# Kernel optimization log

Measured on AMD Instinct MI355X. Metric: run time of the kernel, lower is better.

Reference implementation:

```python
import jax, jax.numpy as jnp
import numpy as np

S, B, H = 2048, 1, 1024
N_HEADS = 16
HEAD_DIM = H // N_HEADS
E, K, F = 8, 2, 2048  # experts, top_k, ffn_hidden
EPS = 1e-5


def layernorm(x, w, b):
    mu = jnp.mean(x, axis=-1, keepdims=True)
    var = jnp.mean(jnp.square(x - mu), axis=-1, keepdims=True)
    return (x - mu) * jax.lax.rsqrt(var + EPS) * w + b


def setup_inputs() -> dict:
    key = jax.random.key(0)
    ks = jax.random.split(key, 8)
    std = 0.02
    return {
        "x": jax.random.normal(ks[0], (S, B, H), dtype=jnp.float32),
        "ln1_w": jnp.ones((H,), jnp.float32),
        "ln1_b": jnp.zeros((H,), jnp.float32),
        "in_proj_w": jax.random.normal(ks[1], (3 * H, H), jnp.float32) * std,
        "in_proj_b": jnp.zeros((3 * H,), jnp.float32),
        "out_proj_w": jax.random.normal(ks[2], (H, H), jnp.float32) * std,
        "out_proj_b": jnp.zeros((H,), jnp.float32),
        "ln2_w": jnp.ones((H,), jnp.float32),
        "ln2_b": jnp.zeros((H,), jnp.float32),
        "router_w": jax.random.normal(ks[3], (E, H), jnp.float32) * std,
        "w1": jax.random.normal(ks[4], (E, H, F), jnp.float32) * std,
        "w2": jax.random.normal(ks[5], (E, F, H), jnp.float32) * std,
    }


def reference(x, ln1_w, ln1_b, in_proj_w, in_proj_b, out_proj_w, out_proj_b,
              ln2_w, ln2_b, router_w, w1, w2):
    s, b, h = x.shape
    # ---- causal self-attention (nn.MultiheadAttention math) ----
    hn = layernorm(x, ln1_w, ln1_b)
    qkv = hn @ in_proj_w.T + in_proj_b          # [S,B,3H]
    q, k, v = jnp.split(qkv, 3, axis=-1)
    q = q.reshape(s, b, N_HEADS, HEAD_DIM)
    k = k.reshape(s, b, N_HEADS, HEAD_DIM)
    v = v.reshape(s, b, N_HEADS, HEAD_DIM)
    scores = jnp.einsum('sbnd,tbnd->bnst', q, k) / np.sqrt(HEAD_DIM)
    causal = jnp.tril(jnp.ones((s, s), bool))
    scores = jnp.where(causal[None, None], scores, -jnp.inf)
    probs = jax.nn.softmax(scores, axis=-1)
    attn = jnp.einsum('bnst,tbnd->sbnd', probs, v).reshape(s, b, h)
    attn = attn @ out_proj_w.T + out_proj_b
    x1 = x + attn
    # ---- dMoE FFN: router softmax -> top-k gates -> expert GELU MLP ----
    hn2 = layernorm(x1, ln2_w, ln2_b).reshape(s * b, h)   # tokens [T,H]
    logits = hn2 @ router_w.T                              # [T,E]
    rp = jax.nn.softmax(logits, axis=-1)
    topw, topi = jax.lax.top_k(rp, K)                      # [T,K]
    gates = jnp.sum(jax.nn.one_hot(topi, E, dtype=hn2.dtype) * topw[..., None], axis=1)  # [T,E]
    hmid = jax.nn.gelu(jnp.einsum('th,ehf->tef', hn2, w1), approximate=False)  # [T,E,F]
    y = jnp.einsum('tef,efh->th', hmid * gates[:, :, None], w2)                # [T,H]
    return x1 + y.reshape(s, b, h)
```

## Files before the change

kernel.cpp:

```cpp
#include <hip/hip_runtime.h>

#define SL 2048
#define HID 1024
#define NHEAD 16
#define HD 64
#define NEXP 8
#define FF 2048
#define MAXTILE 40
#define MAXROWS (MAXTILE * 128)
#define CPAD 32

typedef short bf16x8 __attribute__((ext_vector_type(8)));
typedef float f32x4 __attribute__((ext_vector_type(4)));
typedef unsigned u32x4 __attribute__((ext_vector_type(4)));

__device__ __forceinline__ unsigned short f2bf(float f) {
  unsigned u = __builtin_bit_cast(unsigned, f);
  u += 0x7fffu + ((u >> 16) & 1u);
  return (unsigned short)(u >> 16);
}

__device__ __forceinline__ void gload16(const void* g, void* l) {
  __builtin_amdgcn_global_load_lds((const __attribute__((address_space(1))) void*)g,
                                   (__attribute__((address_space(3))) void*)l,
                                   16, 0, 0);
}

__device__ __forceinline__ void xcd_remap(int& bx, int& by) {
  const int nx = gridDim.x;
  const int nwg = nx * gridDim.y;
  const int L = by * nx + bx;
  const int per = nwg >> 3;
  const int Lp = (L & 7) * per + (L >> 3);
  bx = Lp % nx;
  by = Lp / nx;
}

#define PIPE_WAIT(i, NT)                                                     \
  if ((i) == (NT) - 1)                                                       \
    asm volatile("s_waitcnt vmcnt(0) lgkmcnt(0)" ::: "memory");              \
  else                                                                       \
    asm volatile("s_waitcnt vmcnt(4) lgkmcnt(0)" ::: "memory");              \
  __builtin_amdgcn_s_barrier();

#define GEMM_FRAGS_MFMA(CC)                                                  \
  bf16x8 af[4], bfr[4];                                                      \
  _Pragma("unroll")                                                          \
  for (int mt = 0; mt < 4; mt++)                                             \
    af[mt] = *reinterpret_cast<const bf16x8*>(                               \
        &Asm[CC][(wm + mt * 16 + la) * 32 + lk]);                            \
  _Pragma("unroll")                                                          \
  for (int nt = 0; nt < 4; nt++)                                             \
    bfr[nt] = *reinterpret_cast<const bf16x8*>(                              \
        &Bsm[CC][(wn + nt * 16 + la) * 32 + lk]);                            \
  __builtin_amdgcn_s_setprio(1);                                             \
  _Pragma("unroll")                                                          \
  for (int mt = 0; mt < 4; mt++)                                             \
    _Pragma("unroll")                                                        \
    for (int nt = 0; nt < 4; nt++)                                           \
      acc[mt][nt] =                                                          \
          __builtin_amdgcn_mfma_f32_16x16x32_bf16(af[mt], bfr[nt], acc[mt][nt], 0, 0, 0); \
  __builtin_amdgcn_s_setprio(0);

#define PIPE_ROT()                                                           \
  cc = (cc == 2) ? 0 : cc + 1;                                               \
  cs = (cs == 2) ? 0 : cs + 1;

template <int MODE>
__global__ __launch_bounds__(256) void gemm_bt(
    const unsigned short* __restrict__ A, const unsigned short* __restrict__ Bt,
    int M, int N, int Kstride, int Kloop,
    const float* __restrict__ bias,
    float* __restrict__ outf,
    unsigned short* __restrict__ q_out, unsigned short* __restrict__ k_out,
    unsigned short* __restrict__ vt_out)
{
  __shared__ unsigned short Asm[3][128 * 32];
  __shared__ unsigned short Bsm[3][128 * 32];
  int bx = blockIdx.x, by = blockIdx.y;
  xcd_remap(bx, by);
  const int tid = threadIdx.x;
  const int wave = tid >> 6;
  const int lane = tid & 63;
  const int m0 = by * 128;
  const int n0 = bx * 128;
  const int koff = blockIdx.z * Kloop;
  const int wm = (wave >> 1) * 64;
  const int wn = (wave & 1) * 64;
  const int la = lane & 15;
  const int lk = (lane >> 4) * 8;

  f32x4 acc[4][4] = {};

  const int srow = tid >> 2;
  const int skoff = (tid & 3) * 8;
  const unsigned short* Ag = A + (size_t)(m0 + srow) * Kstride + koff + skoff;
  const unsigned short* Bg = Bt + (size_t)(n0 + srow) * Kstride + koff + skoff;

  auto stage = [&](int s, int k0) {
    gload16(Ag + k0, &Asm[s][wave * 512]);
    gload16(Ag + (size_t)64 * Kstride + k0, &Asm[s][2048 + wave * 512]);
    gload16(Bg + k0, &Bsm[s][wave * 512]);
    gload16(Bg + (size_t)64 * Kstride + k0, &Bsm[s][2048 + wave * 512]);
  };

  stage(0, 0);
  stage(1, 32);
  const int NT = Kloop >> 5;
  int cc = 0, cs = 2;
  for (int i = 0; i < NT; ++i) {
    PIPE_WAIT(i, NT)
    if (i + 2 < NT) stage(cs, (i + 2) << 5);
    GEMM_FRAGS_MFMA(cc)
    PIPE_ROT()
  }

  const int lg = lane >> 4;
#pragma unroll
  for (int mt = 0; mt < 4; mt++) {
#pragma unroll
    for (int nt = 0; nt < 4; nt++) {
#pragma unroll
      for (int r = 0; r < 4; r++) {
        const int row = m0 + wm + mt * 16 + lg * 4 + r;
        const int col = n0 + wn + nt * 16 + la;
        float v = acc[mt][nt][r];
        if (MODE == 0) {
          v += bias[col];
          const int hh = (col & 1023) >> 6;
          const int dd = col & 63;
          const unsigned short bv = f2bf(v);
          if (col < 1024)
            q_out[(size_t)hh * SL * HD + (size_t)row * HD + dd] = bv;
          else if (col < 2048)
            k_out[(size_t)hh * SL * HD + (size_t)row * HD + dd] = bv;
          else
            vt_out[(size_t)hh * HD * SL + (size_t)dd * SL + row] = bv;
        } else {
          outf[(size_t)blockIdx.z * SL * HID + (size_t)row * HID + col] = v;
        }
      }
    }
  }
}

__global__ __launch_bounds__(256) void gemm_moe1(
    const unsigned short* __restrict__ A, const unsigned short* __restrict__ w1t,
    const int* __restrict__ perm, const float* __restrict__ gateg,
    const int* __restrict__ texp, const int* __restrict__ trow,
    unsigned short* __restrict__ hmidg)
{
  __shared__ unsigned short Asm[3][128 * 32];
  __shared__ unsigned short Bsm[3][128 * 32];
  int bx = blockIdx.x, by = blockIdx.y;
  xcd_remap(bx, by);
  const int e = texp[by];
  if (e < 0) return;
  const int row0 = trow[by];
  const int tid = threadIdx.x;
  const int wave = tid >> 6;
  const int lane = tid & 63;
  const int n0 = bx * 128;
  const int wm = (wave >> 1) * 64;
  const int wn = (wave & 1) * 64;
  const int la = lane & 15;
  const int lk = (lane >> 4) * 8;
  f32x4 acc[4][4] = {};

  const int srow = tid >> 2;
  const int skoff = (tid & 3) * 8;
  const int p0 = perm[row0 + srow];
  const int p1 = perm[row0 + 64 + srow];
  const unsigned short* Ag0 = A + (size_t)(p0 < 0 ? 0 : (p0 >> 1)) * HID + skoff;
  const unsigned short* Ag1 = A + (size_t)(p1 < 0 ? 0 : (p1 >> 1)) * HID + skoff;
  const unsigned short* Bg = w1t + (size_t)e * HID * FF + (size_t)(n0 + srow) * HID + skoff;

  auto stage = [&](int s, int k0) {
    gload16(Ag0 + k0, &Asm[s][wave * 512]);
    gload16(Ag1 + k0, &Asm[s][2048 + wave * 512]);
    gload16(Bg + k0, &Bsm[s][wave * 512]);
    gload16(Bg + (size_t)64 * HID + k0, &Bsm[s][2048 + wave * 512]);
  };

  stage(0, 0);
  stage(1, 32);
  const int NT = HID >> 5;
  int cc = 0, cs = 2;
  for (int i = 0; i < NT; ++i) {
    PIPE_WAIT(i, NT)
    if (i + 2 < NT) stage(cs, (i + 2) << 5);
    GEMM_FRAGS_MFMA(cc)
    PIPE_ROT()
  }

  const int lg = lane >> 4;
#pragma unroll
  for (int mt = 0; mt < 4; mt++) {
    float gr[4];
#pragma unroll
    for (int r = 0; r < 4; r++) gr[r] = gateg[row0 + wm + mt * 16 + lg * 4 + r];
#pragma unroll
    for (int nt = 0; nt < 4; nt++) {
#pragma unroll
      for (int r = 0; r < 4; r++) {
        const int grow = row0 + wm + mt * 16 + lg * 4 + r;
        const int col = n0 + wn + nt * 16 + la;
        const float v = acc[mt][nt][r];
        const float g = 0.5f * v * (1.0f + erff(v * 0.70710678118f));
        hmidg[(size_t)grow * FF + col] = f2bf(g * gr[r]);
      }
    }
  }
}

__global__ __launch_bounds__(256) void gemm_moe2(
    const unsigned short* __restrict__ A, const unsigned short* __restrict__ w2t,
    const int* __restrict__ perm,
    const int* __restrict__ texp, const int* __restrict__ trow,
    float* __restrict__ ybuf)
{
  __shared__ unsigned short Asm[3][128 * 32];
  __shared__ unsigned short Bsm[3][128 * 32];
  int bx = blockIdx.x, by = blockIdx.y;
  xcd_remap(bx, by);
  const int e = texp[by];
  if (e < 0) return;
  const int row0 = trow[by];
  const int tid = threadIdx.x;
  const int wave = tid >> 6;
  const int lane = tid & 63;
  const int n0 = bx * 128;
  const int koff = blockIdx.z * (FF / 2);
  const int wm = (wave >> 1) * 64;
  const int wn = (wave & 1) * 64;
  const int la = lane & 15;
  const int lk = (lane >> 4) * 8;
  f32x4 acc[4][4] = {};

  const int srow = tid >> 2;
  const int skoff = (tid & 3) * 8;
  const unsigned short* Ag = A + (size_t)(row0 + srow) * FF + koff + skoff;
  const unsigned short* Bg = w2t + (size_t)e * FF * HID + (size_t)(n0 + srow) * FF + koff + skoff;

  auto stage = [&](int s, int k0) {
    gload16(Ag + k0, &Asm[s][wave * 512]);
    gload16(Ag + (size_t)64 * FF + k0, &Asm[s][2048 + wave * 512]);
    gload16(Bg + k0, &Bsm[s][wave * 512]);
    gload16(Bg + (size_t)64 * FF + k0, &Bsm[s][2048 + wave * 512]);
  };

  stage(0, 0);
  stage(1, 32);
  const int NT = (FF / 2) >> 5;
  int cc = 0, cs = 2;
  for (int i = 0; i < NT; ++i) {
    PIPE_WAIT(i, NT)
    if (i + 2 < NT) stage(cs, (i + 2) << 5);
    GEMM_FRAGS_MFMA(cc)
    PIPE_ROT()
  }

  const int lg = lane >> 4;
#pragma unroll
  for (int mt = 0; mt < 4; mt++) {
    int pr[4];
#pragma unroll
    for (int r = 0; r < 4; r++) pr[r] = perm[row0 + wm + mt * 16 + lg * 4 + r];
#pragma unroll
    for (int nt = 0; nt < 4; nt++) {
#pragma unroll
      for (int r = 0; r < 4; r++) {
        const int p = pr[r];
        if (p >= 0) {
          const int col = n0 + wn + nt * 16 + la;
          ybuf[(size_t)(blockIdx.z * 2 + (p & 1)) * SL * HID + (size_t)(p >> 1) * HID + col] =
              acc[mt][nt][r];
        }
      }
    }
  }
}

__global__ __launch_bounds__(256) void ln_kernel(
    const float* __restrict__ x, const float* __restrict__ w, const float* __restrict__ b,
    unsigned short* __restrict__ ob)
{
  const int row = blockIdx.x;
  const int tid = threadIdx.x;
  const float4 v = *reinterpret_cast<const float4*>(&x[(size_t)row * HID + tid * 4]);
  float s = v.x + v.y + v.z + v.w;
  float q = v.x * v.x + v.y * v.y + v.z * v.z + v.w * v.w;
  for (int off = 32; off > 0; off >>= 1) {
    s += __shfl_down(s, off);
    q += __shfl_down(q, off);
  }
  __shared__ float ps[4], pq[4];
  const int wave = tid >> 6, lane = tid & 63;
  if (lane == 0) { ps[wave] = s; pq[wave] = q; }
  __syncthreads();
  s = ps[0] + ps[1] + ps[2] + ps[3];
  q = pq[0] + pq[1] + pq[2] + pq[3];
  const float mu = s * (1.0f / HID);
  const float inv = rsqrtf(q * (1.0f / HID) - mu * mu + 1e-5f);
  const int i = tid * 4;
  const float4 wv = *reinterpret_cast<const float4*>(&w[i]);
  const float4 bv = *reinterpret_cast<const float4*>(&b[i]);
  ushort4 u;
  u.x = f2bf((v.x - mu) * inv * wv.x + bv.x);
  u.y = f2bf((v.y - mu) * inv * wv.y + bv.y);
  u.z = f2bf((v.z - mu) * inv * wv.z + bv.z);
  u.w = f2bf((v.w - mu) * inv * wv.w + bv.w);
  *reinterpret_cast<ushort4*>(&ob[(size_t)row * HID + i]) = u;
}

__global__ __launch_bounds__(256) void combine_ln(
    const float4* __restrict__ x, const float* __restrict__ bias,
    const float4* __restrict__ p0, const float4* __restrict__ p1,
    float4* __restrict__ x1,
    const float* __restrict__ w, const float* __restrict__ b,
    unsigned short* __restrict__ ob, float* __restrict__ of)
{
  const int row = blockIdx.x;
  const int tid = threadIdx.x;
  const int i4 = row * 256 + tid;
  const int i = tid * 4;
  const float4 bv0 = *reinterpret_cast<const float4*>(&bias[i]);
  const float4 a = x[i4], c = p0[i4], d = p1[i4];
  float4 v;
  v.x = a.x + bv0.x + c.x + d.x;
  v.y = a.y + bv0.y + c.y + d.y;
  v.z = a.z + bv0.z + c.z + d.z;
  v.w = a.w + bv0.w + c.w + d.w;
  x1[i4] = v;
  float s = v.x + v.y + v.z + v.w;
  float q = v.x * v.x + v.y * v.y + v.z * v.z + v.w * v.w;
  for (int off = 32; off > 0; off >>= 1) {
    s += __shfl_down(s, off);
    q += __shfl_down(q, off);
  }
  __shared__ float ps[4], pq[4];
  const int wave = tid >> 6, lane = tid & 63;
  if (lane == 0) { ps[wave] = s; pq[wave] = q; }
  __syncthreads();
  s = ps[0] + ps[1] + ps[2] + ps[3];
  q = pq[0] + pq[1] + pq[2] + pq[3];
  const float mu = s * (1.0f / HID);
  const float inv = rsqrtf(q * (1.0f / HID) - mu * mu + 1e-5f);
  const float4 wv = *reinterpret_cast<const float4*>(&w[i]);
  const float4 bv = *reinterpret_cast<const float4*>(&b[i]);
  const float o0 = (v.x - mu) * inv * wv.x + bv.x;
  const float o1 = (v.y - mu) * inv * wv.y + bv.y;
  const float o2 = (v.z - mu) * inv * wv.z + bv.z;
  const float o3 = (v.w - mu) * inv * wv.w + bv.w;
  ushort4 u; u.x = f2bf(o0); u.y = f2bf(o1); u.z = f2bf(o2); u.w = f2bf(o3);
  *reinterpret_cast<ushort4*>(&ob[(size_t)row * HID + i]) = u;
  float4 o; o.x = o0; o.y = o1; o.z = o2; o.w = o3;
  *reinterpret_cast<float4*>(&of[(size_t)row * HID + i]) = o;
}

__global__ __launch_bounds__(256) void transpose_all(
    const float* __restrict__ w1, const float* __restrict__ w2,
    unsigned short* __restrict__ w1t, unsigned short* __restrict__ w2t)
{
  __shared__ unsigned lt[128 * 66];
  const int z = blockIdx.z;
  const float* in;
  unsigned short* out;
  int R, C, r0, c0;
  if (z < 8) {
    in = w1 + (size_t)z * HID * FF;  out = w1t + (size_t)z * HID * FF;
    R = HID; C = FF;  r0 = blockIdx.y * 128;  c0 = blockIdx.x * 128;
  } else {
    in = w2 + (size_t)(z - 8) * FF * HID;  out = w2t + (size_t)(z - 8) * FF * HID;
    R = FF; C = HID;  r0 = blockIdx.x * 128;  c0 = blockIdx.y * 128;
  }
  const int tid = threadIdx.x;
#pragma unroll
  for (int it = 0; it < 8; it++) {
    const int idx = it * 256 + tid;
    const int rp = idx >> 5;
    const int c4 = (idx & 31) * 4;
    const int r = rp * 2;
    const float4 v0 = *reinterpret_cast<const float4*>(&in[(size_t)(r0 + r) * C + c0 + c4]);
    const float4 v1 = *reinterpret_cast<const float4*>(&in[(size_t)(r0 + r + 1) * C + c0 + c4]);
    const int s = ((c4 >> 2) & 7) << 1;
    const int ri = rp ^ s;
    lt[(c4 + 0) * 66 + ri] = (unsigned)f2bf(v0.x) | ((unsigned)f2bf(v1.x) << 16);
    lt[(c4 + 1) * 66 + ri] = (unsigned)f2bf(v0.y) | ((unsigned)f2bf(v1.y) << 16);
    lt[(c4 + 2) * 66 + ri] = (unsigned)f2bf(v0.z) | ((unsigned)f2bf(v1.z) << 16);
    lt[(c4 + 3) * 66 + ri] = (unsigned)f2bf(v0.w) | ((unsigned)f2bf(v1.w) << 16);
  }
  __syncthreads();
#pragma unroll
  for (int it = 0; it < 16; it++) {
    const int idx = it * 256 + tid;
    const int c = idx >> 5;
    const int r4 = (idx & 31) * 4;
    const int s = ((c >> 2) & 7) << 1;
    const unsigned u0 = lt[c * 66 + ((r4 >> 1) ^ s)];
    const unsigned u1 = lt[c * 66 + (((r4 >> 1) + 1) ^ s)];
    ushort4 u;
    u.x = (unsigned short)(u0 & 0xffff);
    u.y = (unsigned short)(u0 >> 16);
    u.z = (unsigned short)(u1 & 0xffff);
    u.w = (unsigned short)(u1 >> 16);
    *reinterpret_cast<ushort4*>(&out[(size_t)(c0 + c) * R + r0 + r4]) = u;
  }
}

__global__ __launch_bounds__(256) void conv_bf16_2(
    const float4* __restrict__ a, const float4* __restrict__ b,
    ushort4* __restrict__ oa, ushort4* __restrict__ ob, int na4, int nb4)
{
  const int i = blockIdx.x * 256 + threadIdx.x;
  if (i < na4) {
    const float4 v = a[i];
    ushort4 u; u.x = f2bf(v.x); u.y = f2bf(v.y); u.z = f2bf(v.z); u.w = f2bf(v.w);
    oa[i] = u;
  } else if (i - na4 < nb4) {
    const float4 v = b[i - na4];
    ushort4 u; u.x = f2bf(v.x); u.y = f2bf(v.y); u.z = f2bf(v.z); u.w = f2bf(v.w);
    ob[i - na4] = u;
  }
}

__global__ __launch_bounds__(256) void router_kernel(
    const float* __restrict__ hn2f, const float* __restrict__ rw,
    int* __restrict__ ti, float* __restrict__ tg, int* __restrict__ cnt)
{
  __shared__ float wlds[NEXP * HID];
  __shared__ int lcnt[NEXP];
  const int tid = threadIdx.x;
#pragma unroll
  for (int i = 0; i < 8; i++)
    *reinterpret_cast<float4*>(&wlds[i * 1024 + tid * 4]) =
        *reinterpret_cast<const float4*>(&rw[i * 1024 + tid * 4]);
  if (tid < NEXP) lcnt[tid] = 0;
  __syncthreads();

  const int wave = tid >> 6, lane = tid & 63;
#pragma unroll 1
  for (int k = 0; k < 4; k++) {
    const int t = blockIdx.x * 16 + wave * 4 + k;
    float4 xr[4];
#pragma unroll
    for (int c = 0; c < 4; c++)
      xr[c] = *reinterpret_cast<const float4*>(&hn2f[(size_t)t * HID + c * 256 + lane * 4]);
    float p[NEXP];
#pragma unroll
    for (int e = 0; e < NEXP; e++) {
      float s = 0.f;
#pragma unroll
      for (int c = 0; c < 4; c++) {
        const float4 wv = *reinterpret_cast<const float4*>(&wlds[e * 1024 + c * 256 + lane * 4]);
        s += xr[c].x * wv.x + xr[c].y * wv.y + xr[c].z * wv.z + xr[c].w * wv.w;
      }
      s += __shfl_xor(s, 32);
      s += __shfl_xor(s, 16);
      s += __shfl_xor(s, 8);
      s += __shfl_xor(s, 4);
      s += __shfl_xor(s, 2);
      s += __shfl_xor(s, 1);
      p[e] = s;
    }
    if (lane == 0) {
      float mx = p[0];
#pragma unroll
      for (int e = 1; e < NEXP; e++) mx = fmaxf(mx, p[e]);
      float Z = 0.f;
#pragma unroll
      for (int e = 0; e < NEXP; e++) { p[e] = expf(p[e] - mx); Z += p[e]; }
      const float invZ = 1.f / Z;
      int i1 = 0;
#pragma unroll
      for (int e = 1; e < NEXP; e++) if (p[e] > p[i1]) i1 = e;
      int i2 = (i1 == 0) ? 1 : 0;
#pragma unroll
      for (int e = 0; e < NEXP; e++) if (e != i1 && p[e] > p[i2]) i2 = e;
      ti[2 * t] = i1; ti[2 * t + 1] = i2;
      tg[2 * t] = p[i1] * invZ; tg[2 * t + 1] = p[i2] * invZ;
      atomicAdd(&lcnt[i1], 1);
      atomicAdd(&lcnt[i2], 1);
    }
  }
  __syncthreads();
  if (tid < NEXP && lcnt[tid] > 0) atomicAdd(&cnt[tid * CPAD], lcnt[tid]);
}

__global__ void scan_kernel(const int* __restrict__ cnt, int* __restrict__ poff,
                            int* __restrict__ texp, int* __restrict__ trow)
{
  if (threadIdx.x == 0 && blockIdx.x == 0) {
    int off = 0, nt = 0;
    for (int e = 0; e < NEXP; e++) {
      poff[e] = off;
      const int c = cnt[e * CPAD];
      const int ntl = (c + 127) >> 7;
      for (int i = 0; i < ntl; i++) { texp[nt] = e; trow[nt] = off + i * 128; nt++; }
      off += ntl * 128;
    }
    for (int i = nt; i < MAXTILE; i++) { texp[i] = -1; trow[i] = 0; }
  }
}

__global__ __launch_bounds__(256) void build_kernel(
    const int* __restrict__ ti, const float* __restrict__ tg,
    const int* __restrict__ poff, int* __restrict__ fill,
    int* __restrict__ perm, float* __restrict__ gateg)
{
  __shared__ int lcnt[NEXP], lbase[NEXP];
  const int tid = threadIdx.x;
  if (tid < NEXP) lcnt[tid] = 0;
  __syncthreads();
  const int t = blockIdx.x * 256 + tid;
  int e0 = ti[2 * t], e1 = ti[2 * t + 1];
  int l0 = atomicAdd(&lcnt[e0], 1);
  int l1 = atomicAdd(&lcnt[e1], 1);
  __syncthreads();
  if (tid < NEXP) lbase[tid] = (lcnt[tid] > 0) ? atomicAdd(&fill[tid * CPAD], lcnt[tid]) : 0;
  __syncthreads();
  int pos0 = poff[e0] + lbase[e0] + l0;
  int pos1 = poff[e1] + lbase[e1] + l1;
  perm[pos0] = 2 * t;
  gateg[pos0] = tg[2 * t];
  perm[pos1] = 2 * t + 1;
  gateg[pos1] = tg[2 * t + 1];
}

__global__ __launch_bounds__(256) void final_add(
    const float4* __restrict__ x1, const float4* __restrict__ y0,
    const float4* __restrict__ y1, const float4* __restrict__ y2,
    const float4* __restrict__ y3, float4* __restrict__ out)
{
  const int i = blockIdx.x * 256 + threadIdx.x;
  const float4 a = x1[i], b = y0[i], c = y1[i], d = y2[i], e = y3[i];
  float4 o;
  o.x = a.x + b.x + c.x + d.x + e.x;
  o.y = a.y + b.y + c.y + d.y + e.y;
  o.z = a.z + b.z + c.z + d.z + e.z;
  o.w = a.w + b.w + c.w + d.w + e.w;
  out[i] = o;
}

#define SC2 0.1803368801111204f
#define PPITCH 20
__global__ __launch_bounds__(512) void attn_kernel(
    const unsigned short* __restrict__ qb, const unsigned short* __restrict__ kb,
    const unsigned short* __restrict__ vtb, unsigned short* __restrict__ attn)
{
  const int h = blockIdx.y;
  const int tid = threadIdx.x;
  const int wave = tid >> 6, lane = tid & 63;
  const int grp = wave >> 2;
  const int w4 = wave & 3;
  const int la = lane & 15, lg = lane >> 4;
  const int la7 = la & 7;
  __shared__ unsigned short Kt[2][2][64 * 64];
  __shared__ unsigned short Vt[2][2][64 * 64];
  __shared__ unsigned plds[8 * 32 * PPITCH];
  const unsigned short* qh = qb + (size_t)h * SL * HD;
  const unsigned short* kh = kb + (size_t)h * SL * HD;
  const unsigned short* vh = vtb + (size_t)h * HD * SL;
  unsigned* pu = &plds[wave * 32 * PPITCH];

  const int sr_lo = w4 * 8 + (lane >> 3);
  const int ss = lane & 7;

  auto stageKV = [&](int t, int buf) {
    const int kvb = t * 64;
#pragma unroll
    for (int j = 0; j < 2; j++) {
      const int row = j * 32 + sr_lo;
      const int s = ss ^ (row & 7);
      gload16(kh + (size_t)(kvb + row) * HD + s * 8, &Kt[grp][buf][j * 2048 + w4 * 512]);
      gload16(vh + (size_t)row * SL + kvb + s * 8, &Vt[grp][buf][j * 2048 + w4 * 512]);
    }
  };

  for (int half = 0; half < 2; half++) {
    const int qt = half ? (31 - blockIdx.x) : blockIdx.x;
    const int m0 = qt * 64 + w4 * 16;
    const int T = qt + 1;
    const int S = (T + 1) >> 1;
    const int q = m0 + la;

    bf16x8 aq0 = *reinterpret_cast<const bf16x8*>(&qh[(size_t)(m0 + la) * HD + lg * 8]);
    bf16x8 aq1 = *reinterpret_cast<const bf16x8*>(&qh[(size_t)(m0 + la) * HD + 32 + lg * 8]);

    f32x4 oacc[4] = {};
    float mrun = -1e30f, lrun = 0.f;

    if (grp < T) stageKV(grp, 0);
    __syncthreads();
    int cur = 0;

    for (int s = 0; s < S; s++) {
      const int tmy = 2 * s + grp;
      if (tmy + 2 < T) stageKV(tmy + 2, cur ^ 1);
      if (tmy < T) {
        const int kv0 = tmy * 64;
        const unsigned short* Kb = Kt[grp][cur];
        const unsigned short* Vb = Vt[grp][cur];

        f32x4 sac[4] = {};
        __builtin_amdgcn_s_setprio(1);
#pragma unroll
        for (int nt = 0; nt < 4; nt++) {
          const int row = nt * 16 + la;
          bf16x8 b0 = *reinterpret_cast<const bf16x8*>(&Kb[row * 64 + ((lg ^ la7) << 3)]);
          bf16x8 b1 = *reinterpret_cast<const bf16x8*>(&Kb[row * 64 + (((4 + lg) ^ la7) << 3)]);
          sac[nt] = __builtin_amdgcn_mfma_f32_16x16x32_bf16(b0, aq0, sac[nt], 0, 0, 0);
          sac[nt] = __builtin_amdgcn_mfma_f32_16x16x32_bf16(b1, aq1, sac[nt], 0, 0, 0);
        }
        __builtin_amdgcn_s_setprio(0);
        float sv[4][4];
        const bool diag = (tmy == qt);
#pragma unroll
        for (int nt = 0; nt < 4; nt++)
#pragma unroll
          for (int r = 0; r < 4; r++) {
            float xs = sac[nt][r] * SC2;
            if (diag && (kv0 + nt * 16 + lg * 4 + r) > q) xs = -1e30f;
            sv[nt][r] = xs;
          }
        float pm = fmaxf(fmaxf(sv[0][0], sv[0][1]), fmaxf(sv[0][2], sv[0][3]));
#pragma unroll
        for (int nt = 1; nt < 4; nt++)
          pm = fmaxf(pm, fmaxf(fmaxf(sv[nt][0], sv[nt][1]), fmaxf(sv[nt][2], sv[nt][3])));
        pm = fmaxf(pm, __shfl_xor(pm, 16));
        pm = fmaxf(pm, __shfl_xor(pm, 32));
        const float mn = fmaxf(mrun, pm);
        float rs = 0.f;
#pragma unroll
        for (int nt = 0; nt < 4; nt++)
#pragma unroll
          for (int r = 0; r < 4; r++) {
            const float pe = exp2f(sv[nt][r] - mn);
            sv[nt][r] = pe;
            rs += pe;
          }
        rs += __shfl_xor(rs, 16);
        rs += __shfl_xor(rs, 32);
        if (__ballot(pm > mrun) != 0ULL) {
          const float al = exp2f(mrun - mn);
#pragma unroll
          for (int dt = 0; dt < 4; dt++)
#pragma unroll
            for (int r = 0; r < 4; r++) oacc[dt][r] *= al;
          lrun = lrun * al + rs;
          mrun = mn;
        } else {
          lrun += rs;
        }
#pragma unroll
        for (int nt = 0; nt < 4; nt++)
#pragma unroll
          for (int rp = 0; rp < 2; rp++) {
            unsigned pk;
            asm("v_cvt_pk_bf16_f32 %0, %1, %2"
                : "=v"(pk) : "v"(sv[nt][rp * 2]), "v"(sv[nt][rp * 2 + 1]));
            pu[(nt * 8 + lg * 2 + rp) * PPITCH + la] = pk;
          }
        asm volatile("s_waitcnt lgkmcnt(0)" ::: "memory");
        __builtin_amdgcn_sched_barrier(0);
        u32x4 w0, w1;
#pragma unroll
        for (int jj = 0; jj < 4; jj++) {
          w0[jj] = pu[(lg * 4 + jj) * PPITCH + la];
          w1[jj] = pu[(16 + lg * 4 + jj) * PPITCH + la];
        }
        const bf16x8 pa0 = __builtin_bit_cast(bf16x8, w0);
        const bf16x8 pa1 = __builtin_bit_cast(bf16x8, w1);
        __builtin_amdgcn_s_setprio(1);
#pragma unroll
        for (int dt = 0; dt < 4; dt++) {
          const int row = dt * 16 + la;
          bf16x8 v0 = *reinterpret_cast<const bf16x8*>(&Vb[row * 64 + ((lg ^ la7) << 3)]);
          bf16x8 v1 = *reinterpret_cast<const bf16x8*>(&Vb[row * 64 + (((4 + lg) ^ la7) << 3)]);
          oacc[dt] = __builtin_amdgcn_mfma_f32_16x16x32_bf16(v0, pa0, oacc[dt], 0, 0, 0);
          oacc[dt] = __builtin_amdgcn_mfma_f32_16x16x32_bf16(v1, pa1, oacc[dt], 0, 0, 0);
        }
        __builtin_amdgcn_s_setprio(0);
      }
      __syncthreads();
      cur ^= 1;
    }

    float* xb = (float*)&Kt[0][0][0];
    float* mlb = (float*)&Vt[0][0][0];
    if (grp == 1) {
#pragma unroll
      for (int dt = 0; dt < 4; dt++)
#pragma unroll
        for (int r = 0; r < 4; r++)
          xb[w4 * 1024 + (dt * 16 + lg * 4 + r) * 16 + la] = oacc[dt][r];
      if (lg == 0) {
        mlb[w4 * 32 + la * 2] = mrun;
        mlb[w4 * 32 + la * 2 + 1] = lrun;
      }
    }
    __syncthreads();
    if (grp == 0) {
      const float m1 = mlb[w4 * 32 + la * 2];
      const float l1 = mlb[w4 * 32 + la * 2 + 1];
      const float mm = fmaxf(mrun, m1);
      const float a0 = exp2f(mrun - mm);
      const float a1 = exp2f(m1 - mm);
      const float linv = 1.0f / (lrun * a0 + l1 * a1);
#pragma unroll
      for (int dt = 0; dt < 4; dt++) {
        ushort4 u;
        float o0 = (oacc[dt][0] * a0 + xb[w4 * 1024 + (dt * 16 + lg * 4 + 0) * 16 + la] * a1) * linv;
        float o1 = (oacc[dt][1] * a0 + xb[w4 * 1024 + (dt * 16 + lg * 4 + 1) * 16 + la] * a1) * linv;
        float o2 = (oacc[dt][2] * a0 + xb[w4 * 1024 + (dt * 16 + lg * 4 + 2) * 16 + la] * a1) * linv;
        float o3 = (oacc[dt][3] * a0 + xb[w4 * 1024 + (dt * 16 + lg * 4 + 3) * 16 + la] * a1) * linv;
        u.x = f2bf(o0); u.y = f2bf(o1); u.z = f2bf(o2); u.w = f2bf(o3);
        *reinterpret_cast<ushort4*>(&attn[(size_t)q * HID + h * HD + dt * 16 + lg * 4]) = u;
      }
    }
    __syncthreads();
  }
}

extern "C" void kernel_launch(void* const* d_in, const int* in_sizes, int n_in,
                              void* d_out, int out_size, void* d_ws, size_t ws_size,
                              hipStream_t stream)
{
  const float* x          = (const float*)d_in[0];
  const float* ln1_w      = (const float*)d_in[1];
  const float* ln1_b      = (const float*)d_in[2];
  const float* in_proj_w  = (const float*)d_in[3];
  const float* in_proj_b  = (const float*)d_in[4];
  const float* out_proj_w = (const float*)d_in[5];
  const float* out_proj_b = (const float*)d_in[6];
  const float* ln2_w      = (const float*)d_in[7];
  const float* ln2_b      = (const float*)d_in[8];
  const float* router_w   = (const float*)d_in[9];
  const float* w1         = (const float*)d_in[10];
  const float* w2         = (const float*)d_in[11];
  float* out = (float*)d_out;

  char* ws = (char*)d_ws;
  size_t off = 0;
  auto alloc = [&](size_t bytes) -> void* {
    void* p = ws + off;
    off += (bytes + 255) & ~(size_t)255;
    return p;
  };
  unsigned short* hn_b   = (unsigned short*)alloc((size_t)SL * HID * 2);
  unsigned short* ipw_b  = (unsigned short*)alloc((size_t)3 * HID * HID * 2);
  unsigned short* opw_b  = (unsigned short*)alloc((size_t)HID * HID * 2);
  unsigned short* qb     = (unsigned short*)alloc((size_t)SL * HID * 2);
  unsigned short* kb     = (unsigned short*)alloc((size_t)SL * HID * 2);
  unsigned short* vtb    = (unsigned short*)alloc((size_t)SL * HID * 2);
  unsigned short* attn_b = (unsigned short*)alloc((size_t)SL * HID * 2);
  float*          x1     = (float*)alloc((size_t)SL * HID * 4);
  float*          pbuf   = (float*)alloc((size_t)2 * SL * HID * 4);
  unsigned short* hn2_b  = (unsigned short*)alloc((size_t)SL * HID * 2);
  float*          hn2_f  = (float*)alloc((size_t)SL * HID * 4);
  unsigned short* w1t    = (unsigned short*)alloc((size_t)NEXP * HID * FF * 2);
  unsigned short* w2t    = (unsigned short*)alloc((size_t)NEXP * HID * FF * 2);
  unsigned short* hmidg  = (unsigned short*)alloc((size_t)MAXROWS * FF * 2);
  float*          ybuf   = (float*)alloc((size_t)4 * SL * HID * 4);
  int*            ti     = (int*)alloc((size_t)SL * 2 * 4);
  float*          tg     = (float*)alloc((size_t)SL * 2 * 4);
  int*            perm   = (int*)alloc((size_t)MAXROWS * 4);
  float*          gateg  = (float*)alloc((size_t)MAXROWS * 4);
  int*            cnt    = (int*)alloc(NEXP * CPAD * 4);
  int*            fill   = (int*)alloc(NEXP * CPAD * 4);
  int*            poff   = (int*)alloc(64 * 4);
  int*            texp   = (int*)alloc(64 * 4);
  int*            trow   = (int*)alloc(64 * 4);

  const dim3 blk(256);

  hipMemsetAsync(cnt, 0, NEXP * CPAD * 4, stream);
  hipMemsetAsync(fill, 0, NEXP * CPAD * 4, stream);
  hipMemsetAsync(perm, 0xFF, (size_t)MAXROWS * 4, stream);
  hipMemsetAsync(gateg, 0, (size_t)MAXROWS * 4, stream);

  conv_bf16_2<<<4096, blk, 0, stream>>>(
      (const float4*)in_proj_w, (const float4*)out_proj_w,
      (ushort4*)ipw_b, (ushort4*)opw_b, 3 * HID * HID / 4, HID * HID / 4);
  transpose_all<<<dim3(16, 8, 16), blk, 0, stream>>>(w1, w2, w1t, w2t);

  ln_kernel<<<SL, blk, 0, stream>>>(x, ln1_w, ln1_b, hn_b);

  gemm_bt<0><<<dim3(3 * HID / 128, SL / 128), blk, 0, stream>>>(
      hn_b, ipw_b, SL, 3 * HID, HID, HID,
      in_proj_b, nullptr, qb, kb, vtb);

  attn_kernel<<<dim3(16, NHEAD), dim3(512), 0, stream>>>(qb, kb, vtb, attn_b);

  gemm_bt<2><<<dim3(HID / 128, SL / 128, 2), blk, 0, stream>>>(
      attn_b, opw_b, SL, HID, HID, HID / 2,
      nullptr, pbuf, nullptr, nullptr, nullptr);

  combine_ln<<<SL, blk, 0, stream>>>(
      (const float4*)x, out_proj_b, (const float4*)pbuf,
      (const float4*)(pbuf + (size_t)SL * HID), (float4*)x1,
      ln2_w, ln2_b, hn2_b, hn2_f);

  router_kernel<<<SL / 16, blk, 0, stream>>>(hn2_f, router_w, ti, tg, cnt);
  scan_kernel<<<1, 64, 0, stream>>>(cnt, poff, texp, trow);
  build_kernel<<<SL / 256, blk, 0, stream>>>(ti, tg, poff, fill, perm, gateg);

  gemm_moe1<<<dim3(FF / 128, MAXTILE), blk, 0, stream>>>(
      hn2_b, w1t, perm, gateg, texp, trow, hmidg);
  gemm_moe2<<<dim3(HID / 128, MAXTILE, 2), blk, 0, stream>>>(
      hmidg, w2t, perm, texp, trow, ybuf);

  final_add<<<SL * HID / 1024, blk, 0, stream>>>(
      (const float4*)x1, (const float4*)ybuf,
      (const float4*)(ybuf + (size_t)SL * HID),
      (const float4*)(ybuf + (size_t)2 * SL * HID),
      (const float4*)(ybuf + (size_t)3 * SL * HID),
      (float4*)out);
}
```

Baseline: 266.1 us.

## Fuse weight conversion into LN1 and expert transpose into QKV GEMM launch

```diff
diff --git a/kernel.cpp b/kernel.cpp
--- a/kernel.cpp
+++ b/kernel.cpp
@@ -66,14 +66,137 @@
   cc = (cc == 2) ? 0 : cc + 1;                                               \
   cs = (cs == 2) ? 0 : cs + 1;
 
+__global__ __launch_bounds__(256) void qkv_trans_kernel(
+    const unsigned short* __restrict__ A, const unsigned short* __restrict__ Bt,
+    const float* __restrict__ bias,
+    unsigned short* __restrict__ q_out, unsigned short* __restrict__ k_out,
+    unsigned short* __restrict__ vt_out,
+    const float* __restrict__ w1, const float* __restrict__ w2,
+    unsigned short* __restrict__ w1t, unsigned short* __restrict__ w2t)
+{
+  __shared__ union {
+    struct { unsigned short A[3][4096]; unsigned short B[3][4096]; } g;
+    unsigned lt[128 * 66];
+  } sm;
+  const int tid = threadIdx.x;
+
+  if (blockIdx.z == 0) {
+    unsigned short (*Asm)[4096] = sm.g.A;
+    unsigned short (*Bsm)[4096] = sm.g.B;
+    int bx = blockIdx.x, by = blockIdx.y;
+    xcd_remap(bx, by);
+    const int wave = tid >> 6;
+    const int lane = tid & 63;
+    const int m0 = by * 128;
+    const int n0 = bx * 128;
+    const int wm = (wave >> 1) * 64;
+    const int wn = (wave & 1) * 64;
+    const int la = lane & 15;
+    const int lk = (lane >> 4) * 8;
+
+    f32x4 acc[4][4] = {};
+
+    const int srow = tid >> 2;
+    const int skoff = (tid & 3) * 8;
+    const unsigned short* Ag = A + (size_t)(m0 + srow) * HID + skoff;
+    const unsigned short* Bg = Bt + (size_t)(n0 + srow) * HID + skoff;
+
+    auto stage = [&](int s, int k0) {
+      gload16(Ag + k0, &Asm[s][wave * 512]);
+      gload16(Ag + (size_t)64 * HID + k0, &Asm[s][2048 + wave * 512]);
+      gload16(Bg + k0, &Bsm[s][wave * 512]);
+      gload16(Bg + (size_t)64 * HID + k0, &Bsm[s][2048 + wave * 512]);
+    };
+
+    stage(0, 0);
+    stage(1, 32);
+    const int NT = HID >> 5;
+    int cc = 0, cs = 2;
+    for (int i = 0; i < NT; ++i) {
+      PIPE_WAIT(i, NT)
+      if (i + 2 < NT) stage(cs, (i + 2) << 5);
+      GEMM_FRAGS_MFMA(cc)
+      PIPE_ROT()
+    }
+
+    const int lg = lane >> 4;
+#pragma unroll
+    for (int mt = 0; mt < 4; mt++) {
+#pragma unroll
+      for (int nt = 0; nt < 4; nt++) {
+#pragma unroll
+        for (int r = 0; r < 4; r++) {
+          const int row = m0 + wm + mt * 16 + lg * 4 + r;
+          const int col = n0 + wn + nt * 16 + la;
+          float v = acc[mt][nt][r] + bias[col];
+          const int hh = (col & 1023) >> 6;
+          const int dd = col & 63;
+          const unsigned short bv = f2bf(v);
+          if (col < 1024)
+            q_out[(size_t)hh * SL * HD + (size_t)row * HD + dd] = bv;
+          else if (col < 2048)
+            k_out[(size_t)hh * SL * HD + (size_t)row * HD + dd] = bv;
+          else
+            vt_out[(size_t)hh * HD * SL + (size_t)dd * SL + row] = bv;
+        }
+      }
+    }
+  } else {
+    const int id = blockIdx.y * 24 + blockIdx.x;
+    if (id >= 256) return;
+    const int tx = id & 15;
+    const int ty = (id >> 4) & 7;
+    const int tz = ((int)blockIdx.z - 1) * 2 + (id >> 7);
+    const float* in;
+    unsigned short* out;
+    int R, C, r0, c0;
+    if (tz < 8) {
+      in = w1 + (size_t)tz * HID * FF;  out = w1t + (size_t)tz * HID * FF;
+      R = HID; C = FF;  r0 = ty * 128;  c0 = tx * 128;
+    } else {
+      in = w2 + (size_t)(tz - 8) * FF * HID;  out = w2t + (size_t)(tz - 8) * FF * HID;
+      R = FF; C = HID;  r0 = tx * 128;  c0 = ty * 128;
+    }
+#pragma unroll
+    for (int it = 0; it < 8; it++) {
+      const int idx = it * 256 + tid;
+      const int rp = idx >> 5;
+      const int c4 = (idx & 31) * 4;
+      const int r = rp * 2;
+      const float4 v0 = *reinterpret_cast<const float4*>(&in[(size_t)(r0 + r) * C + c0 + c4]);
+      const float4 v1 = *reinterpret_cast<const float4*>(&in[(size_t)(r0 + r + 1) * C + c0 + c4]);
+      const int s = ((c4 >> 2) & 7) << 1;
+      const int ri = rp ^ s;
+      sm.lt[(c4 + 0) * 66 + ri] = (unsigned)f2bf(v0.x) | ((unsigned)f2bf(v1.x) << 16);
+      sm.lt[(c4 + 1) * 66 + ri] = (unsigned)f2bf(v0.y) | ((unsigned)f2bf(v1.y) << 16);
+      sm.lt[(c4 + 2) * 66 + ri] = (unsigned)f2bf(v0.z) | ((unsigned)f2bf(v1.z) << 16);
+      sm.lt[(c4 + 3) * 66 + ri] = (unsigned)f2bf(v0.w) | ((unsigned)f2bf(v1.w) << 16);
+    }
+    __syncthreads();
+#pragma unroll
+    for (int it = 0; it < 16; it++) {
+      const int idx = it * 256 + tid;
+      const int c = idx >> 5;
+      const int r4 = (idx & 31) * 4;
+      const int s = ((c >> 2) & 7) << 1;
+      const unsigned u0 = sm.lt[c * 66 + ((r4 >> 1) ^ s)];
+      const unsigned u1 = sm.lt[c * 66 + (((r4 >> 1) + 1) ^ s)];
+      ushort4 u;
+      u.x = (unsigned short)(u0 & 0xffff);
+      u.y = (unsigned short)(u0 >> 16);
+      u.z = (unsigned short)(u1 & 0xffff);
+      u.w = (unsigned short)(u1 >> 16);
+      *reinterpret_cast<ushort4*>(&out[(size_t)(c0 + c) * R + r0 + r4]) = u;
+    }
+  }
+}
+
 template <int MODE>
 __global__ __launch_bounds__(256) void gemm_bt(
     const unsigned short* __restrict__ A, const unsigned short* __restrict__ Bt,
     int M, int N, int Kstride, int Kloop,
     const float* __restrict__ bias,
-    float* __restrict__ outf,
-    unsigned short* __restrict__ q_out, unsigned short* __restrict__ k_out,
-    unsigned short* __restrict__ vt_out)
+    float* __restrict__ outf)
 {
   __shared__ unsigned short Asm[3][128 * 32];
   __shared__ unsigned short Bsm[3][128 * 32];
@@ -124,21 +247,7 @@
       for (int r = 0; r < 4; r++) {
         const int row = m0 + wm + mt * 16 + lg * 4 + r;
         const int col = n0 + wn + nt * 16 + la;
-        float v = acc[mt][nt][r];
-        if (MODE == 0) {
-          v += bias[col];
-          const int hh = (col & 1023) >> 6;
-          const int dd = col & 63;
-          const unsigned short bv = f2bf(v);
-          if (col < 1024)
-            q_out[(size_t)hh * SL * HD + (size_t)row * HD + dd] = bv;
-          else if (col < 2048)
-            k_out[(size_t)hh * SL * HD + (size_t)row * HD + dd] = bv;
-          else
-            vt_out[(size_t)hh * HD * SL + (size_t)dd * SL + row] = bv;
-        } else {
-          outf[(size_t)blockIdx.z * SL * HID + (size_t)row * HID + col] = v;
-        }
+        outf[(size_t)blockIdx.z * SL * HID + (size_t)row * HID + col] = acc[mt][nt][r];
       }
     }
   }
@@ -281,36 +390,53 @@
   }
 }
 
-__global__ __launch_bounds__(256) void ln_kernel(
+__global__ __launch_bounds__(256) void ln_conv_kernel(
     const float* __restrict__ x, const float* __restrict__ w, const float* __restrict__ b,
-    unsigned short* __restrict__ ob)
-{
-  const int row = blockIdx.x;
+    unsigned short* __restrict__ ob,
+    const float4* __restrict__ cva, const float4* __restrict__ cvb,
+    ushort4* __restrict__ coa, ushort4* __restrict__ cob)
+{
   const int tid = threadIdx.x;
-  const float4 v = *reinterpret_cast<const float4*>(&x[(size_t)row * HID + tid * 4]);
-  float s = v.x + v.y + v.z + v.w;
-  float q = v.x * v.x + v.y * v.y + v.z * v.z + v.w * v.w;
-  for (int off = 32; off > 0; off >>= 1) {
-    s += __shfl_down(s, off);
-    q += __shfl_down(q, off);
-  }
-  __shared__ float ps[4], pq[4];
-  const int wave = tid >> 6, lane = tid & 63;
-  if (lane == 0) { ps[wave] = s; pq[wave] = q; }
-  __syncthreads();
-  s = ps[0] + ps[1] + ps[2] + ps[3];
-  q = pq[0] + pq[1] + pq[2] + pq[3];
-  const float mu = s * (1.0f / HID);
-  const float inv = rsqrtf(q * (1.0f / HID) - mu * mu + 1e-5f);
-  const int i = tid * 4;
-  const float4 wv = *reinterpret_cast<const float4*>(&w[i]);
-  const float4 bv = *reinterpret_cast<const float4*>(&b[i]);
-  ushort4 u;
-  u.x = f2bf((v.x - mu) * inv * wv.x + bv.x);
-  u.y = f2bf((v.y - mu) * inv * wv.y + bv.y);
-  u.z = f2bf((v.z - mu) * inv * wv.z + bv.z);
-  u.w = f2bf((v.w - mu) * inv * wv.w + bv.w);
-  *reinterpret_cast<ushort4*>(&ob[(size_t)row * HID + i]) = u;
+  if ((int)blockIdx.x < SL) {
+    const int row = blockIdx.x;
+    const float4 v = *reinterpret_cast<const float4*>(&x[(size_t)row * HID + tid * 4]);
+    float s = v.x + v.y + v.z + v.w;
+    float q = v.x * v.x + v.y * v.y + v.z * v.z + v.w * v.w;
+    for (int off = 32; off > 0; off >>= 1) {
+      s += __shfl_down(s, off);
+      q += __shfl_down(q, off);
+    }
+    __shared__ float ps[4], pq[4];
+    const int wave = tid >> 6, lane = tid & 63;
+    if (lane == 0) { ps[wave] = s; pq[wave] = q; }
+    __syncthreads();
+    s = ps[0] + ps[1] + ps[2] + ps[3];
+    q = pq[0] + pq[1] + pq[2] + pq[3];
+    const float mu = s * (1.0f / HID);
+    const float inv = rsqrtf(q * (1.0f / HID) - mu * mu + 1e-5f);
+    const int i = tid * 4;
+    const float4 wv = *reinterpret_cast<const float4*>(&w[i]);
+    const float4 bv = *reinterpret_cast<const float4*>(&b[i]);
+    ushort4 u;
+    u.x = f2bf((v.x - mu) * inv * wv.x + bv.x);
+    u.y = f2bf((v.y - mu) * inv * wv.y + bv.y);
+    u.z = f2bf((v.z - mu) * inv * wv.z + bv.z);
+    u.w = f2bf((v.w - mu) * inv * wv.w + bv.w);
+    *reinterpret_cast<ushort4*>(&ob[(size_t)row * HID + i]) = u;
+  } else {
+    const int NA = 3 * HID * HID / 4, NB = HID * HID / 4;
+    for (int i = ((int)blockIdx.x - SL) * 256 + tid; i < NA + NB; i += 512 * 256) {
+      if (i < NA) {
+        const float4 v = cva[i];
+        ushort4 u; u.x = f2bf(v.x); u.y = f2bf(v.y); u.z = f2bf(v.z); u.w = f2bf(v.w);
+        coa[i] = u;
+      } else {
+        const float4 v = cvb[i - NA];
+        ushort4 u; u.x = f2bf(v.x); u.y = f2bf(v.y); u.z = f2bf(v.z); u.w = f2bf(v.w);
+        cob[i - NA] = u;
+      }
+    }
+  }
 }
 
 __global__ __launch_bounds__(256) void combine_ln(
@@ -356,72 +482,6 @@
   *reinterpret_cast<ushort4*>(&ob[(size_t)row * HID + i]) = u;
   float4 o; o.x = o0; o.y = o1; o.z = o2; o.w = o3;
   *reinterpret_cast<float4*>(&of[(size_t)row * HID + i]) = o;
-}
-
-__global__ __launch_bounds__(256) void transpose_all(
-    const float* __restrict__ w1, const float* __restrict__ w2,
-    unsigned short* __restrict__ w1t, unsigned short* __restrict__ w2t)
-{
-  __shared__ unsigned lt[128 * 66];
-  const int z = blockIdx.z;
-  const float* in;
-  unsigned short* out;
-  int R, C, r0, c0;
-  if (z < 8) {
-    in = w1 + (size_t)z * HID * FF;  out = w1t + (size_t)z * HID * FF;
-    R = HID; C = FF;  r0 = blockIdx.y * 128;  c0 = blockIdx.x * 128;
-  } else {
-    in = w2 + (size_t)(z - 8) * FF * HID;  out = w2t + (size_t)(z - 8) * FF * HID;
-    R = FF; C = HID;  r0 = blockIdx.x * 128;  c0 = blockIdx.y * 128;
-  }
-  const int tid = threadIdx.x;
-#pragma unroll
-  for (int it = 0; it < 8; it++) {
-    const int idx = it * 256 + tid;
-    const int rp = idx >> 5;
-    const int c4 = (idx & 31) * 4;
-    const int r = rp * 2;
-    const float4 v0 = *reinterpret_cast<const float4*>(&in[(size_t)(r0 + r) * C + c0 + c4]);
-    const float4 v1 = *reinterpret_cast<const float4*>(&in[(size_t)(r0 + r + 1) * C + c0 + c4]);
-    const int s = ((c4 >> 2) & 7) << 1;
-    const int ri = rp ^ s;
-    lt[(c4 + 0) * 66 + ri] = (unsigned)f2bf(v0.x) | ((unsigned)f2bf(v1.x) << 16);
-    lt[(c4 + 1) * 66 + ri] = (unsigned)f2bf(v0.y) | ((unsigned)f2bf(v1.y) << 16);
-    lt[(c4 + 2) * 66 + ri] = (unsigned)f2bf(v0.z) | ((unsigned)f2bf(v1.z) << 16);
-    lt[(c4 + 3) * 66 + ri] = (unsigned)f2bf(v0.w) | ((unsigned)f2bf(v1.w) << 16);
-  }
-  __syncthreads();
-#pragma unroll
-  for (int it = 0; it < 16; it++) {
-    const int idx = it * 256 + tid;
-    const int c = idx >> 5;
-    const int r4 = (idx & 31) * 4;
-    const int s = ((c >> 2) & 7) << 1;
-    const unsigned u0 = lt[c * 66 + ((r4 >> 1) ^ s)];
-    const unsigned u1 = lt[c * 66 + (((r4 >> 1) + 1) ^ s)];
-    ushort4 u;
-    u.x = (unsigned short)(u0 & 0xffff);
-    u.y = (unsigned short)(u0 >> 16);
-    u.z = (unsigned short)(u1 & 0xffff);
-    u.w = (unsigned short)(u1 >> 16);
-    *reinterpret_cast<ushort4*>(&out[(size_t)(c0 + c) * R + r0 + r4]) = u;
-  }
-}
-
-__global__ __launch_bounds__(256) void conv_bf16_2(
-    const float4* __restrict__ a, const float4* __restrict__ b,
-    ushort4* __restrict__ oa, ushort4* __restrict__ ob, int na4, int nb4)
-{
-  const int i = blockIdx.x * 256 + threadIdx.x;
-  if (i < na4) {
-    const float4 v = a[i];
-    ushort4 u; u.x = f2bf(v.x); u.y = f2bf(v.y); u.z = f2bf(v.z); u.w = f2bf(v.w);
-    oa[i] = u;
-  } else if (i - na4 < nb4) {
-    const float4 v = b[i - na4];
-    ushort4 u; u.x = f2bf(v.x); u.y = f2bf(v.y); u.z = f2bf(v.z); u.w = f2bf(v.w);
-    ob[i - na4] = u;
-  }
 }
 
 __global__ __launch_bounds__(256) void router_kernel(
@@ -779,22 +839,19 @@
   hipMemsetAsync(perm, 0xFF, (size_t)MAXROWS * 4, stream);
   hipMemsetAsync(gateg, 0, (size_t)MAXROWS * 4, stream);
 
-  conv_bf16_2<<<4096, blk, 0, stream>>>(
+  ln_conv_kernel<<<SL + 512, blk, 0, stream>>>(
+      x, ln1_w, ln1_b, hn_b,
       (const float4*)in_proj_w, (const float4*)out_proj_w,
-      (ushort4*)ipw_b, (ushort4*)opw_b, 3 * HID * HID / 4, HID * HID / 4);
-  transpose_all<<<dim3(16, 8, 16), blk, 0, stream>>>(w1, w2, w1t, w2t);
-
-  ln_kernel<<<SL, blk, 0, stream>>>(x, ln1_w, ln1_b, hn_b);
-
-  gemm_bt<0><<<dim3(3 * HID / 128, SL / 128), blk, 0, stream>>>(
-      hn_b, ipw_b, SL, 3 * HID, HID, HID,
-      in_proj_b, nullptr, qb, kb, vtb);
+      (ushort4*)ipw_b, (ushort4*)opw_b);
+
+  qkv_trans_kernel<<<dim3(3 * HID / 128, SL / 128, 9), blk, 0, stream>>>(
+      hn_b, ipw_b, in_proj_b, qb, kb, vtb, w1, w2, w1t, w2t);
 
   attn_kernel<<<dim3(16, NHEAD), dim3(512), 0, stream>>>(qb, kb, vtb, attn_b);
 
   gemm_bt<2><<<dim3(HID / 128, SL / 128, 2), blk, 0, stream>>>(
       attn_b, opw_b, SL, HID, HID, HID / 2,
-      nullptr, pbuf, nullptr, nullptr, nullptr);
+      out_proj_b, pbuf);
 
   combine_ln<<<SL, blk, 0, stream>>>(
       (const float4*)x, out_proj_b, (const float4*)pbuf,
```

After: 257.3 us. 3.3% less time.
